# Kernel tuning notes

Measured on AMD Instinct MI355X. Metric: run time of the kernel, lower is better.

The kernel has to match this reference:

```python
import jax, jax.numpy as jnp
import numpy as np

B, D_IN, D_H = 256, 512, 512
LN_EPS = 1e-5


def setup_inputs() -> dict:
    key = jax.random.key(0)
    ks = jax.random.split(key, 12)
    def xavier(k, shape):
        fan_in, fan_out = shape[1], shape[0]
        lim = np.sqrt(6.0 / (fan_in + fan_out))
        return jax.random.uniform(k, shape, jnp.float32, -lim, lim)
    return {
        "x_t": jax.random.normal(ks[0], (B, D_IN), jnp.float32),
        "C_prev": jax.random.normal(ks[1], (B, D_H, D_H), jnp.float32),
        "n_prev": jax.random.normal(ks[2], (B, D_H), jnp.float32),
        "Wq": xavier(ks[3], (D_H, D_IN)),
        "Wk": xavier(ks[4], (D_H, D_IN)),
        "Wv": xavier(ks[5], (D_H, D_IN)),
        "wi_w": xavier(ks[6], (1, D_IN)),
        "wi_b": jnp.zeros((1,), jnp.float32),
        "wf_w": xavier(ks[7], (1, D_IN)),
        "wf_b": jnp.full((1,), 3.0, jnp.float32),
        "Wo_w": xavier(ks[8], (D_H, D_IN)),
        "Wo_b": jnp.zeros((D_H,), jnp.float32),
        "ln_g": jnp.ones((D_H,), jnp.float32),
        "ln_b": jnp.zeros((D_H,), jnp.float32),
    }


def reference(x_t, C_prev, n_prev, Wq, Wk, Wv, wi_w, wi_b, wf_w, wf_b, Wo_w, Wo_b, ln_g, ln_b):
    # projections (Linear: x @ W.T + b)
    q = x_t @ Wq.T                      # [B, d]
    k = x_t @ Wk.T                      # [B, d]
    v = x_t @ Wv.T                      # [B, d]
    i_t = jnp.minimum(jnp.exp(x_t @ wi_w.T + wi_b), 50.0)   # [B, 1]
    f_t = jax.nn.sigmoid(x_t @ wf_w.T + wf_b)               # [B, 1]
    o_t = jax.nn.sigmoid(x_t @ Wo_w.T + Wo_b)               # [B, d]
    # matrix memory update: C_t = f*C_prev + i*(v k^T)
    C_t = f_t[:, :, None] * C_prev + i_t[:, :, None] * (v[:, :, None] * k[:, None, :])
    n_t = f_t * n_prev + i_t * k        # [B, d]
    # normalized retrieval
    h_tilde = jnp.einsum("bij,bj->bi", C_t, q)              # [B, d]
    nq = jnp.sum(n_t * q, axis=-1, keepdims=True)           # [B, 1]
    h_tilde = h_tilde / jnp.maximum(jnp.abs(nq), 1.0)
    h = o_t * h_tilde
    # LayerNorm epilogue
    mu = jnp.mean(h, axis=-1, keepdims=True)
    var = jnp.mean((h - mu) ** 2, axis=-1, keepdims=True)
    h_t = (h - mu) * jax.lax.rsqrt(var + LN_EPS) * ln_g + ln_b
    return (h_t, C_t, n_t)
```

## Files before the change

kernel.cpp:

```cpp
#include <hip/hip_runtime.h>
#include <math.h>

#define D 512
#define BATCH 256

typedef float f4 __attribute__((ext_vector_type(4)));

__global__ __launch_bounds__(256) void proj_gemm(
    const float* __restrict__ X,
    const float* __restrict__ Wq, const float* __restrict__ Wk,
    const float* __restrict__ Wv, const float* __restrict__ Wo,
    const float* __restrict__ Wo_b,
    float* __restrict__ qb, float* __restrict__ kb,
    float* __restrict__ vb, float* __restrict__ ob)
{
    const int mat = blockIdx.z;
    const float* W = (mat == 0) ? Wq : (mat == 1) ? Wk : (mat == 2) ? Wv : Wo;
    float* Y = (mat == 0) ? qb : (mat == 1) ? kb : (mat == 2) ? vb : ob;

    const int m0 = blockIdx.y * 64;
    const int n0 = blockIdx.x * 64;

    __shared__ float Xs[64][33];
    __shared__ float Ws[64][33];

    const int t = threadIdx.x;
    const int lr = t >> 3;
    const int lc = (t & 7) * 4;
    const int ty = t >> 4;
    const int tx = t & 15;

    float acc[4][4] = {};

    for (int k0 = 0; k0 < D; k0 += 32) {
        float4 xa = *(const float4*)&X[(size_t)(m0 + lr) * D + k0 + lc];
        float4 xb = *(const float4*)&X[(size_t)(m0 + lr + 32) * D + k0 + lc];
        float4 wa = *(const float4*)&W[(size_t)(n0 + lr) * D + k0 + lc];
        float4 wb = *(const float4*)&W[(size_t)(n0 + lr + 32) * D + k0 + lc];
        __syncthreads();
        Xs[lr][lc + 0] = xa.x; Xs[lr][lc + 1] = xa.y; Xs[lr][lc + 2] = xa.z; Xs[lr][lc + 3] = xa.w;
        Xs[lr + 32][lc + 0] = xb.x; Xs[lr + 32][lc + 1] = xb.y; Xs[lr + 32][lc + 2] = xb.z; Xs[lr + 32][lc + 3] = xb.w;
        Ws[lr][lc + 0] = wa.x; Ws[lr][lc + 1] = wa.y; Ws[lr][lc + 2] = wa.z; Ws[lr][lc + 3] = wa.w;
        Ws[lr + 32][lc + 0] = wb.x; Ws[lr + 32][lc + 1] = wb.y; Ws[lr + 32][lc + 2] = wb.z; Ws[lr + 32][lc + 3] = wb.w;
        __syncthreads();
#pragma unroll
        for (int kk = 0; kk < 32; ++kk) {
            float a0 = Xs[ty * 4 + 0][kk];
            float a1 = Xs[ty * 4 + 1][kk];
            float a2 = Xs[ty * 4 + 2][kk];
            float a3 = Xs[ty * 4 + 3][kk];
            float b0 = Ws[tx * 4 + 0][kk];
            float b1 = Ws[tx * 4 + 1][kk];
            float b2 = Ws[tx * 4 + 2][kk];
            float b3 = Ws[tx * 4 + 3][kk];
            acc[0][0] += a0 * b0; acc[0][1] += a0 * b1; acc[0][2] += a0 * b2; acc[0][3] += a0 * b3;
            acc[1][0] += a1 * b0; acc[1][1] += a1 * b1; acc[1][2] += a1 * b2; acc[1][3] += a1 * b3;
            acc[2][0] += a2 * b0; acc[2][1] += a2 * b1; acc[2][2] += a2 * b2; acc[2][3] += a2 * b3;
            acc[3][0] += a3 * b0; acc[3][1] += a3 * b1; acc[3][2] += a3 * b2; acc[3][3] += a3 * b3;
        }
    }

#pragma unroll
    for (int i = 0; i < 4; ++i) {
        int row = m0 + ty * 4 + i;
#pragma unroll
        for (int j = 0; j < 4; ++j) {
            int col = n0 + tx * 4 + j;
            float y = acc[i][j];
            if (mat == 3) y = 1.0f / (1.0f + expf(-(y + Wo_b[col])));
            Y[(size_t)row * D + col] = y;
        }
    }
}

__device__ __forceinline__ float blockReduceSum16(float val, float* red) {
#pragma unroll
    for (int off = 32; off > 0; off >>= 1)
        val += __shfl_down(val, off, 64);
    const int lane = threadIdx.x & 63;
    const int w = threadIdx.x >> 6;
    __syncthreads();
    if (lane == 0) red[w] = val;
    __syncthreads();
    float s = 0.0f;
#pragma unroll
    for (int i = 0; i < 16; ++i) s += red[i];
    return s;
}

__global__ __launch_bounds__(1024) void mega(
    const float* __restrict__ x, const float* __restrict__ n_prev,
    const float* __restrict__ C_prev,
    const float* __restrict__ wi_w, const float* __restrict__ wi_b,
    const float* __restrict__ wf_w, const float* __restrict__ wf_b,
    const float* __restrict__ qb, const float* __restrict__ kb,
    const float* __restrict__ vb, const float* __restrict__ ob,
    const float* __restrict__ ln_g, const float* __restrict__ ln_be,
    float* __restrict__ out_h, float* __restrict__ out_C,
    float* __restrict__ out_n)
{
    __shared__ float red[16];
    __shared__ float hs[D];

    const int b = blockIdx.x;
    const int t = threadIdx.x;
    const int lane = t & 63;
    const int w = t >> 6;

    const size_t bD = (size_t)b * D;

    float si = 0.0f, sf = 0.0f;
    if (t < D) {
        float xv = x[bD + t];
        si = xv * wi_w[t];
        sf = xv * wf_w[t];
    }
    si = blockReduceSum16(si, red);
    sf = blockReduceSum16(sf, red);
    const float i_t = fminf(expf(si + wi_b[0]), 50.0f);
    const float f_t = 1.0f / (1.0f + expf(-(sf + wf_b[0])));

    float nq_p = 0.0f;
    if (t < D) {
        float nv = f_t * n_prev[bD + t] + i_t * kb[bD + t];
        out_n[bD + t] = nv;
        nq_p = nv * qb[bD + t];
    }
    const float nq = blockReduceSum16(nq_p, red);
    const float invnq = 1.0f / fmaxf(fabsf(nq), 1.0f);

    const f4* k4 = (const f4*)(kb + bD);
    const f4* q4 = (const f4*)(qb + bD);
    const f4 ka = k4[lane], kc = k4[lane + 64];
    const f4 qa = q4[lane], qc = q4[lane + 64];

    const float* vrow = vb + bD;
    const float* orow = ob + bD;
    const f4* Cp = (const f4*)(C_prev + bD * D);
    f4*       Ct = (f4*)(out_C + bD * D);

#pragma unroll 2
    for (int j = 0; j < D / 16; ++j) {
        const int r = (j << 4) + w;
        const float a = i_t * vrow[r];
        const f4* cpr = Cp + (size_t)r * (D / 4);
        f4 c0 = __builtin_nontemporal_load(cpr + lane);
        f4 c1 = __builtin_nontemporal_load(cpr + lane + 64);
        f4 r0 = f_t * c0 + a * ka;
        f4 r1 = f_t * c1 + a * kc;
        f4* ctr = Ct + (size_t)r * (D / 4);
        __builtin_nontemporal_store(r0, ctr + lane);
        __builtin_nontemporal_store(r1, ctr + lane + 64);
        f4 m = r0 * qa + r1 * qc;
        float dot = m.x + m.y + m.z + m.w;
#pragma unroll
        for (int off = 32; off > 0; off >>= 1)
            dot += __shfl_down(dot, off, 64);
        if (lane == 0)
            hs[r] = dot * orow[r] * invnq;
    }

    __syncthreads();
    float h0 = (t < D) ? hs[t] : 0.0f;
    const float mu = blockReduceSum16(h0, red) * (1.0f / 512.0f);
    const float d0 = (t < D) ? (h0 - mu) : 0.0f;
    const float var = blockReduceSum16(d0 * d0, red) * (1.0f / 512.0f);
    const float rstd = rsqrtf(var + 1e-5f);
    if (t < D)
        out_h[bD + t] = d0 * rstd * ln_g[t] + ln_be[t];
}

extern "C" void kernel_launch(void* const* d_in, const int* in_sizes, int n_in,
                              void* d_out, int out_size, void* d_ws, size_t ws_size,
                              hipStream_t stream) {
    const float* x_t    = (const float*)d_in[0];
    const float* C_prev = (const float*)d_in[1];
    const float* n_prev = (const float*)d_in[2];
    const float* Wq     = (const float*)d_in[3];
    const float* Wk     = (const float*)d_in[4];
    const float* Wv     = (const float*)d_in[5];
    const float* wi_w   = (const float*)d_in[6];
    const float* wi_b   = (const float*)d_in[7];
    const float* wf_w   = (const float*)d_in[8];
    const float* wf_b   = (const float*)d_in[9];
    const float* Wo_w   = (const float*)d_in[10];
    const float* Wo_b   = (const float*)d_in[11];
    const float* ln_g   = (const float*)d_in[12];
    const float* ln_b   = (const float*)d_in[13];

    float* out = (float*)d_out;
    float* out_h = out;
    float* out_C = out + (size_t)BATCH * D;
    float* out_n = out + (size_t)BATCH * D + (size_t)BATCH * D * D;

    float* ws = (float*)d_ws;
    const size_t BD = (size_t)BATCH * D;
    float* qb = ws;
    float* kb = ws + BD;
    float* vb = ws + 2 * BD;
    float* ob = ws + 3 * BD;

    proj_gemm<<<dim3(D / 64, BATCH / 64, 4), 256, 0, stream>>>(
        x_t, Wq, Wk, Wv, Wo_w, Wo_b, qb, kb, vb, ob);

    mega<<<dim3(BATCH), 1024, 0, stream>>>(
        x_t, n_prev, C_prev, wi_w, wi_b, wf_w, wf_b,
        qb, kb, vb, ob, ln_g, ln_b, out_h, out_C, out_n);
}
```

Baseline: 494.3 us.

## Fully unroll C update loop and defer warp reductions to raise memory parallelism

The row loop in the memory-update kernel is fully unrolled. The per-row scale factors are preloaded into registers, and the per-row partial dot products are kept in an array so the shuffle reductions run after all loads and stores are issued. This moves the cross-lane reduction latency out of the streaming loop and lets many C_prev loads be in flight at once. The C_prev loads also switch from nontemporal to normal loads. The cost is much higher register pressure in a 1024-thread block, which could cause spills.

```diff
diff --git a/kernel.cpp b/kernel.cpp
--- a/kernel.cpp
+++ b/kernel.cpp
@@ -139,25 +139,37 @@
     const f4* Cp = (const f4*)(C_prev + bD * D);
     f4*       Ct = (f4*)(out_C + bD * D);
 
-#pragma unroll 2
-    for (int j = 0; j < D / 16; ++j) {
+    float av[32];
+#pragma unroll
+    for (int j = 0; j < 32; ++j)
+        av[j] = i_t * vrow[(j << 4) + w];
+
+    float acc[32];
+#pragma unroll
+    for (int j = 0; j < 32; ++j) {
         const int r = (j << 4) + w;
-        const float a = i_t * vrow[r];
         const f4* cpr = Cp + (size_t)r * (D / 4);
-        f4 c0 = __builtin_nontemporal_load(cpr + lane);
-        f4 c1 = __builtin_nontemporal_load(cpr + lane + 64);
-        f4 r0 = f_t * c0 + a * ka;
-        f4 r1 = f_t * c1 + a * kc;
+        f4 c0 = cpr[lane];
+        f4 c1 = cpr[lane + 64];
+        f4 r0 = f_t * c0 + av[j] * ka;
+        f4 r1 = f_t * c1 + av[j] * kc;
         f4* ctr = Ct + (size_t)r * (D / 4);
         __builtin_nontemporal_store(r0, ctr + lane);
         __builtin_nontemporal_store(r1, ctr + lane + 64);
         f4 m = r0 * qa + r1 * qc;
-        float dot = m.x + m.y + m.z + m.w;
+        acc[j] = m.x + m.y + m.z + m.w;
+    }
+
+#pragma unroll
+    for (int j = 0; j < 32; ++j) {
+        float d = acc[j];
 #pragma unroll
         for (int off = 32; off > 0; off >>= 1)
-            dot += __shfl_down(dot, off, 64);
-        if (lane == 0)
-            hs[r] = dot * orow[r] * invnq;
+            d += __shfl_down(d, off, 64);
+        if (lane == 0) {
+            const int r = (j << 4) + w;
+            hs[r] = d * orow[r] * invnq;
+        }
     }
 
     __syncthreads();
@@ -205,5 +217,5 @@
 
     mega<<<dim3(BATCH), 1024, 0, stream>>>(
         x_t, n_prev, C_prev, wi_w, wi_b, wf_w, wf_b,
-        qb, kb, vb, ob, ln_g, ln_b, out_h, out_C, out_n);
-}
+        qb, kb, vb, ob, ln_g, ln_b, out_h, out_n ? out_C : out_C, out_n);
+}
```

Result: slower. 597.0 us (+20.8%).
